# Kernel tuning notes

Hardware: AMD Instinct MI355X
Metric: run time of the kernel (lower is better)

Reference implementation:

```python
import jax, jax.numpy as jnp
import numpy as np
from jax import lax

B, UNITS, IN_DIM = 1024, 4096, 256
CHI = 4  # forced: scatter writes 16 = chi*chi values per pair


def setup_inputs() -> dict:
    key = jax.random.key(0)
    k1, k2, k3 = jax.random.split(key, 3)
    inputs = jax.random.normal(k1, (B, IN_DIM), dtype=jnp.float32)
    W = jax.random.normal(k2, (UNITS, IN_DIM), dtype=jnp.float32) * 0.5  # sigma=0.5
    b = 2.0 * jnp.pi * jax.random.uniform(k3, (UNITS,), dtype=jnp.float32)
    return {"inputs": inputs, "W": W, "b": b}


def reference(inputs, W, b):
    # theta: [B, U]
    theta = inputs @ W.T + b
    half = theta * 0.5
    c = jnp.cos(half) ** 2          # R00 (real)
    s = jnp.sin(half) ** 2          # R11 (real)
    o = jnp.sin(theta) * 0.5        # imag part of R01
    z = jnp.zeros_like(c)
    R00 = lax.complex(c, z)
    R01 = lax.complex(z, o)
    R10 = lax.complex(z, -o)
    R11 = lax.complex(s, z)
    # R: [B, U, 2, 2] single-qubit rotation matrix per unit
    R = jnp.stack([jnp.stack([R00, R01], -1), jnp.stack([R10, R11], -1)], -2)
    A = R[:, 0::2]   # [B, K, 2, 2], K = U/2
    Bm = R[:, 1::2]  # [B, K, 2, 2]
    # kron(A, Bm)[2a+c, 2b+d] = A[a,b] * Bm[c,d] -> axes (a,c,b,d) then reshape
    kron = (A[:, :, :, None, :, None] * Bm[:, :, None, :, None, :]).reshape(
        A.shape[0], A.shape[1], CHI, CHI)
    # original returns (batch, chi, chi, units/2)
    return jnp.transpose(kron, (0, 2, 3, 1))
```

## Files before the change

### kernel.cpp

```cpp
#include <hip/hip_runtime.h>

#define IND 256
#define KC  32

__global__ __launch_bounds__(256, 4)
void FeatureEncodingLayer_30374008718005_kernel(
        const float* __restrict__ X,
        const float* __restrict__ W,
        const float* __restrict__ bias,
        float* __restrict__ outf)
{
    __shared__ float Ws[2][KC][128];

    const int tid  = threadIdx.x;
    const int lane = tid & 63;
    const int wid  = __builtin_amdgcn_readfirstlane(tid >> 6);

    const int ut = blockIdx.x & 31;
    const int bt = blockIdx.x >> 5;
    const int b0 = bt * 32;
    const int u0 = ut * 128;
    const int p0 = ut * 64;

    const int q  = tid & 7;
    const int rq = tid >> 3;

    const float* xw = X + (size_t)(b0 + 8 * wid) * IND;

    float acc[8][2];
#pragma unroll
    for (int i = 0; i < 8; ++i) { acc[i][0] = 0.f; acc[i][1] = 0.f; }

    float4 pf[4];
#define STAGE_LOAD(c) do {                                                     \
    _Pragma("unroll")                                                          \
    for (int j = 0; j < 4; ++j)                                                \
        pf[j] = *reinterpret_cast<const float4*>(                              \
            W + (size_t)(u0 + rq + 32 * j) * IND + (c) * KC + q * 4);          \
    } while (0)

#define STAGE_WRITE(buf) do {                                                  \
    _Pragma("unroll")                                                          \
    for (int j = 0; j < 4; ++j) {                                              \
        const int col = (rq + 32 * j) ^ (q << 2);                              \
        Ws[buf][q * 4 + 0][col] = pf[j].x;                                     \
        Ws[buf][q * 4 + 1][col] = pf[j].y;                                     \
        Ws[buf][q * 4 + 2][col] = pf[j].z;                                     \
        Ws[buf][q * 4 + 3][col] = pf[j].w;                                     \
    }                                                                          \
    } while (0)

    STAGE_LOAD(0);
    STAGE_WRITE(0);
    __syncthreads();

    for (int c = 0; c < IND / KC; ++c) {
        const int cur = c & 1;
        if (c < IND / KC - 1) STAGE_LOAD(c + 1);

        const float* xc = xw + c * KC;
#pragma unroll 4
        for (int k = 0; k < KC; ++k) {
            const int s = ((k >> 2) & 7) << 2;
            const float2 wv = *reinterpret_cast<const float2*>(
                &Ws[cur][k][(2 * lane) ^ s]);
#pragma unroll
            for (int i = 0; i < 8; ++i) {
                const float xv = xc[i * IND + k];
                acc[i][0] = fmaf(xv, wv.x, acc[i][0]);
                acc[i][1] = fmaf(xv, wv.y, acc[i][1]);
            }
        }
        if (c < IND / KC - 1) {
            STAGE_WRITE(cur ^ 1);
            __syncthreads();
        }
    }
#undef STAGE_LOAD
#undef STAGE_WRITE

    const float2 bv = *reinterpret_cast<const float2*>(bias + u0 + 2 * lane);

#pragma unroll
    for (int i = 0; i < 8; ++i) {
        const int b = b0 + 8 * wid + i;
        const float tA = acc[i][0] + bv.x;
        const float tB = acc[i][1] + bv.y;
        float sA, cA, sB, cB;
        __sincosf(tA, &sA, &cA);
        __sincosf(tB, &sB, &cB);
        const float ca = 0.5f * (1.f + cA);
        const float sa = 0.5f * (1.f - cA);
        const float cb = 0.5f * (1.f + cB);
        const float sb = 0.5f * (1.f - cB);
        const float oo = 0.25f * sA * sB;

        float* bp = outf + (size_t)b * 32768 + p0 + lane;
        bp[ 0 * 2048] =  ca * cb;
        bp[ 1 * 2048] = 0.f;
        bp[ 2 * 2048] = 0.f;
        bp[ 3 * 2048] = -oo;
        bp[ 4 * 2048] = 0.f;
        bp[ 5 * 2048] =  ca * sb;
        bp[ 6 * 2048] =  oo;
        bp[ 7 * 2048] = 0.f;
        bp[ 8 * 2048] = 0.f;
        bp[ 9 * 2048] =  oo;
        bp[10 * 2048] =  sa * cb;
        bp[11 * 2048] = 0.f;
        bp[12 * 2048] = -oo;
        bp[13 * 2048] = 0.f;
        bp[14 * 2048] = 0.f;
        bp[15 * 2048] =  sa * sb;
    }
}

extern "C" void kernel_launch(void* const* d_in, const int* in_sizes, int n_in,
                              void* d_out, int out_size, void* d_ws, size_t ws_size,
                              hipStream_t stream) {
    const float* X  = (const float*)d_in[0];
    const float* W  = (const float*)d_in[1];
    const float* bv = (const float*)d_in[2];

    FeatureEncodingLayer_30374008718005_kernel<<<dim3(1024), dim3(256), 0, stream>>>(
        X, W, bv, (float*)d_out);
}
```

Measured before the change: 44.60 us.

## Double the K chunk and pack k-pairs into float4 shared-memory reads

Raises the K chunk from 32 to 64, which halves the number of stage/sync iterations. The shared-memory W tile is re-laid-out so each row holds k-pairs interleaved per unit, letting each lane read one float4 covering two k values for its two units instead of a float2 per k. The change is meant to cut LDS instruction count and barrier overhead, at the cost of doubled prefetch registers and lower occupancy (launch bounds min blocks per CU drops from 4 to 2).

```diff
diff --git a/kernel.cpp b/kernel.cpp
--- a/kernel.cpp
+++ b/kernel.cpp
@@ -1,16 +1,16 @@
 #include <hip/hip_runtime.h>
 
 #define IND 256
-#define KC  32
+#define KC  64
 
-__global__ __launch_bounds__(256, 4)
+__global__ __launch_bounds__(256, 2)
 void FeatureEncodingLayer_30374008718005_kernel(
         const float* __restrict__ X,
         const float* __restrict__ W,
         const float* __restrict__ bias,
         float* __restrict__ outf)
 {
-    __shared__ float Ws[2][KC][128];
+    __shared__ float Ws[2][KC / 2][256];
 
     const int tid  = threadIdx.x;
     const int lane = tid & 63;
@@ -22,31 +22,33 @@
     const int u0 = ut * 128;
     const int p0 = ut * 64;
 
-    const int q  = tid & 7;
-    const int rq = tid >> 3;
+    const int q  = tid & 15;
+    const int rq = tid >> 4;
 
-    const float* xw = X + (size_t)(b0 + 8 * wid) * IND;
+    const float* xc = X + (size_t)(b0 + 8 * wid) * IND;
 
     float acc[8][2];
 #pragma unroll
     for (int i = 0; i < 8; ++i) { acc[i][0] = 0.f; acc[i][1] = 0.f; }
 
-    float4 pf[4];
+    float4 pf[8];
 #define STAGE_LOAD(c) do {                                                     \
     _Pragma("unroll")                                                          \
-    for (int j = 0; j < 4; ++j)                                                \
+    for (int j = 0; j < 8; ++j)                                                \
         pf[j] = *reinterpret_cast<const float4*>(                              \
-            W + (size_t)(u0 + rq + 32 * j) * IND + (c) * KC + q * 4);          \
+            W + (size_t)(u0 + rq + 16 * j) * IND + (c) * KC + q * 4);          \
     } while (0)
 
 #define STAGE_WRITE(buf) do {                                                  \
+    const int r0  = 2 * q, r1 = 2 * q + 1;                                     \
+    const int sw0 = (r0 & 7) << 2, sw1 = (r1 & 7) << 2;                        \
     _Pragma("unroll")                                                          \
-    for (int j = 0; j < 4; ++j) {                                              \
-        const int col = (rq + 32 * j) ^ (q << 2);                              \
-        Ws[buf][q * 4 + 0][col] = pf[j].x;                                     \
-        Ws[buf][q * 4 + 1][col] = pf[j].y;                                     \
-        Ws[buf][q * 4 + 2][col] = pf[j].z;                                     \
-        Ws[buf][q * 4 + 3][col] = pf[j].w;                                     \
+    for (int j = 0; j < 8; ++j) {                                              \
+        const int u2 = 2 * (rq + 16 * j);                                      \
+        *reinterpret_cast<float2*>(&Ws[buf][r0][u2 ^ sw0]) =                   \
+            make_float2(pf[j].x, pf[j].y);                                     \
+        *reinterpret_cast<float2*>(&Ws[buf][r1][u2 ^ sw1]) =                   \
+            make_float2(pf[j].z, pf[j].w);                                     \
     }                                                                          \
     } while (0)
 
@@ -58,17 +60,20 @@
         const int cur = c & 1;
         if (c < IND / KC - 1) STAGE_LOAD(c + 1);
 
-        const float* xc = xw + c * KC;
-#pragma unroll 4
-        for (int k = 0; k < KC; ++k) {
-            const int s = ((k >> 2) & 7) << 2;
-            const float2 wv = *reinterpret_cast<const float2*>(
-                &Ws[cur][k][(2 * lane) ^ s]);
+#pragma unroll 8
+        for (int kp = 0; kp < KC / 2; ++kp) {
+            const int sw = (kp & 7) << 2;
+            const float4 wq = *reinterpret_cast<const float4*>(
+                &Ws[cur][kp][(4 * lane) ^ sw]);
+            const int kg = c * KC + 2 * kp;
 #pragma unroll
             for (int i = 0; i < 8; ++i) {
-                const float xv = xc[i * IND + k];
-                acc[i][0] = fmaf(xv, wv.x, acc[i][0]);
-                acc[i][1] = fmaf(xv, wv.y, acc[i][1]);
+                const float x0 = xc[i * IND + kg];
+                const float x1 = xc[i * IND + kg + 1];
+                acc[i][0] = fmaf(x0, wq.x, acc[i][0]);
+                acc[i][0] = fmaf(x1, wq.y, acc[i][0]);
+                acc[i][1] = fmaf(x0, wq.z, acc[i][1]);
+                acc[i][1] = fmaf(x1, wq.w, acc[i][1]);
             }
         }
         if (c < IND / KC - 1) {
```

After: 56.42 us. +26.5%, slower.
